# Kernel optimization log

Measured on AMD Instinct MI355X. Metric: run time of the kernel, lower is better.

Reference implementation:

```python
import jax, jax.numpy as jnp
import numpy as np

E, H, I, T = 8, 1024, 4096, 8192  # experts, hidden, intermediate, total tokens


def setup_inputs() -> dict:
    key = jax.random.key(0)
    k1, k2, k3 = jax.random.split(key, 3)
    hiddens = jax.random.normal(k1, (T, H), dtype=jnp.float32)
    # expert weights, scaled like standard init
    w1_weight = jax.random.normal(k2, (E, H, I), dtype=jnp.float32) * (1.0 / np.sqrt(H).astype(np.float32))
    w2_weight = jax.random.normal(k3, (E, I, H), dtype=jnp.float32) * (1.0 / np.sqrt(I).astype(np.float32))
    # tokens are pre-grouped by expert; equal load of T//E tokens per expert
    batch_sizes = jnp.full((E,), T // E, dtype=jnp.int32)
    return {"hiddens": hiddens, "batch_sizes": batch_sizes,
            "w1_weight": w1_weight, "w2_weight": w2_weight}


def _gmm(x, w, batch_sizes):
    """Grouped matmul: rows of x are grouped contiguously by expert.
    x: [T, K], w: [E, K, N], batch_sizes: [E] (sums to T). Returns [T, N].
    Loop is over the small fixed expert count; each iteration is a dense
    GEMM with rows outside the expert's segment masked to zero.
    """
    n_experts = w.shape[0]
    ends = jnp.cumsum(batch_sizes)
    starts = ends - batch_sizes
    tok = jnp.arange(x.shape[0])[:, None]  # [T, 1]
    out = jnp.zeros((x.shape[0], w.shape[2]), dtype=x.dtype)
    for e in range(n_experts):
        mask = (tok >= starts[e]) & (tok < ends[e])  # [T, 1]
        out = out + jnp.where(mask, x, jnp.zeros((), x.dtype)) @ w[e]
    return out


def reference(hiddens, batch_sizes, w1_weight, w2_weight):
    up = _gmm(hiddens, w1_weight, batch_sizes)    # [T, I]
    down = _gmm(up, w2_weight, batch_sizes)       # [T, H]
    return down
```

## Files before the change

kernel.cpp:

```cpp
#include <hip/hip_runtime.h>
#include <hip/hip_bf16.h>


typedef unsigned short u16;
typedef unsigned int u32;
typedef __attribute__((ext_vector_type(8))) short bf16x8;
typedef __attribute__((ext_vector_type(4))) float f32x4;
typedef __attribute__((ext_vector_type(4))) u32 u32x4;

#define E_N 8
#define H_N 1024
#define I_N 4096
#define T_N 8192

#define GLD2LDS16(g, l)                                                        \
  __builtin_amdgcn_global_load_lds(                                            \
      (const __attribute__((address_space(1))) void*)(g),                      \
      (__attribute__((address_space(3))) void*)(l), 16, 0, 0)

__device__ __forceinline__ u32 pkbf(float lo, float hi) {
  u32 a = __float_as_uint(lo) + 0x8000u;
  u32 b = __float_as_uint(hi) + 0x8000u;
  return __builtin_amdgcn_perm(b, a, 0x07060302u);
}

__device__ __forceinline__ u16 f2bf(float f) {
  __hip_bfloat16 h = __float2bfloat16(f);
  return *(reinterpret_cast<u16*>(&h));
}

__global__ __launch_bounds__(256) void cvt_kernel(const float* __restrict__ src,
                                                  u16* __restrict__ dst) {
  const size_t i = ((size_t)blockIdx.x * 256 + threadIdx.x) * 8;
  float4 a = *(const float4*)(src + i);
  float4 b = *(const float4*)(src + i + 4);
  *(u32x4*)(dst + i) = (u32x4){pkbf(a.x, a.y), pkbf(a.z, a.w),
                               pkbf(b.x, b.y), pkbf(b.z, b.w)};
}

__global__ __launch_bounds__(256) void transp_kernel(const float* __restrict__ w2,
                                                     u16* __restrict__ w2t) {
  __shared__ float tile[64 * 65];
  const int tid = threadIdx.x;
  const int h0 = blockIdx.x * 64;
  const int i0 = blockIdx.y * 64;
  const float* src = w2 + (size_t)blockIdx.z * I_N * H_N;
  u16* dst = w2t + (size_t)blockIdx.z * H_N * I_N;

  {
    const int r = tid >> 4;
    const int c4 = (tid & 15) * 4;
#pragma unroll
    for (int rr = 0; rr < 4; rr++) {
      const int row = rr * 16 + r;
      float4 v = *(const float4*)(src + (size_t)(i0 + row) * H_N + h0 + c4);
      tile[row * 65 + c4 + 0] = v.x;
      tile[row * 65 + c4 + 1] = v.y;
      tile[row * 65 + c4 + 2] = v.z;
      tile[row * 65 + c4 + 3] = v.w;
    }
  }
  __syncthreads();

  {
    const int hr = tid >> 3;
    const int ic = (tid & 7) * 8;
#pragma unroll
    for (int hh = 0; hh < 2; hh++) {
      const int h = hh * 32 + hr;
      u32 p[4];
#pragma unroll
      for (int j = 0; j < 4; j++)
        p[j] = pkbf(tile[(ic + 2 * j) * 65 + h], tile[(ic + 2 * j + 1) * 65 + h]);
      *(u32x4*)(dst + (size_t)(h0 + h) * I_N + i0 + ic) =
          (u32x4){p[0], p[1], p[2], p[3]};
    }
  }
}

__global__ __launch_bounds__(256) void wgemm_kernel(const u16* __restrict__ w2t,
                                                    const u16* __restrict__ w1b,
                                                    u16* __restrict__ mt) {
  __shared__ u16 ldsA[4096];
  __shared__ u16 ldsB[4096];

  const int tid = threadIdx.x;
  const int lane = tid & 63;
  const int wv = tid >> 6;
  const int wm = wv >> 1, wn = wv & 1;
  const int lm = lane & 15, quad = lane >> 4;

  const int e = blockIdx.x >> 6;
  const int t = blockIdx.x & 63;
  const int row0 = (t >> 3) * 128;
  const int col0 = (t & 7) * 128;

  const u16* Ae = w2t + (size_t)e * H_N * I_N;
  const u16* Be = w1b + (size_t)e * H_N * I_N;
  u16* mte = mt + (size_t)e * H_N * H_N;

  const int s_r = tid >> 2;
  const int s_k = (tid & 3) * 8;
  const u16* gA0 = Ae + (size_t)(row0 + s_r) * I_N + s_k;
  const u16* gA1 = gA0 + (size_t)64 * I_N;
  const u16* gB0 = Be + (size_t)(col0 + s_r) * I_N + s_k;
  const u16* gB1 = gB0 + (size_t)64 * I_N;
  u16* ldsA_dst = ldsA + wv * 512;
  u16* ldsB_dst = ldsB + wv * 512;

  f32x4 acc[4][4];
#pragma unroll
  for (int i = 0; i < 4; i++)
#pragma unroll
    for (int j = 0; j < 4; j++) acc[i][j] = (f32x4){0.f, 0.f, 0.f, 0.f};

  for (int k0 = 0; k0 < I_N; k0 += 32) {
    GLD2LDS16(gA0 + k0, ldsA_dst);
    GLD2LDS16(gA1 + k0, ldsA_dst + 2048);
    GLD2LDS16(gB0 + k0, ldsB_dst);
    GLD2LDS16(gB1 + k0, ldsB_dst + 2048);

    __syncthreads();

    bf16x8 af[4], bfr[4];
#pragma unroll
    for (int mi = 0; mi < 4; mi++)
      af[mi] = *(const bf16x8*)(ldsA + (wm * 64 + mi * 16 + lm) * 32 + quad * 8);
#pragma unroll
    for (int ni = 0; ni < 4; ni++)
      bfr[ni] = *(const bf16x8*)(ldsB + (wn * 64 + ni * 16 + lm) * 32 + quad * 8);
#pragma unroll
    for (int mi = 0; mi < 4; mi++)
#pragma unroll
      for (int ni = 0; ni < 4; ni++)
        acc[mi][ni] = __builtin_amdgcn_mfma_f32_16x16x32_bf16(
            af[mi], bfr[ni], acc[mi][ni], 0, 0, 0);

    __syncthreads();
  }

  const int orow = row0 + wm * 64 + quad * 4;
  const int ocol = col0 + wn * 64 + lm;
#pragma unroll
  for (int mi = 0; mi < 4; mi++)
#pragma unroll
    for (int ni = 0; ni < 4; ni++)
#pragma unroll
      for (int r = 0; r < 4; r++)
        mte[(size_t)(orow + mi * 16 + r) * H_N + ocol + ni * 16] =
            f2bf(acc[mi][ni][r]);
}

__global__ __launch_bounds__(256) void tgemm_kernel(const u16* __restrict__ xb,
                                                    const int* __restrict__ bsz,
                                                    const u16* __restrict__ mt,
                                                    float* __restrict__ out) {
  __shared__ u16 ldsA[4096];
  __shared__ u16 ldsB[4096];

  const int tid = threadIdx.x;
  const int lane = tid & 63;
  const int wv = tid >> 6;
  const int wm = wv >> 1, wn = wv & 1;
  const int lm = lane & 15, quad = lane >> 4;

  const int bm = blockIdx.x >> 3, bn = blockIdx.x & 7;
  const int row0 = bm * 128;
  const int col0 = bn * 128;

  int e = 0, start = 0;
#pragma unroll
  for (int i = 0; i < E_N; i++) {
    int b = bsz[i];
    if (row0 >= start + b) { start += b; e = i + 1; }
  }
  const u16* mte = mt + (size_t)e * H_N * H_N;

  const int s_r = tid >> 2;
  const int s_k = (tid & 3) * 8;
  const u16* gA0 = xb + (size_t)(row0 + s_r) * H_N + s_k;
  const u16* gA1 = gA0 + (size_t)64 * H_N;
  const u16* gB0 = mte + (size_t)(col0 + s_r) * H_N + s_k;
  const u16* gB1 = gB0 + (size_t)64 * H_N;
  u16* ldsA_dst = ldsA + wv * 512;
  u16* ldsB_dst = ldsB + wv * 512;

  f32x4 acc[4][4];
#pragma unroll
  for (int i = 0; i < 4; i++)
#pragma unroll
    for (int j = 0; j < 4; j++) acc[i][j] = (f32x4){0.f, 0.f, 0.f, 0.f};

  for (int k0 = 0; k0 < H_N; k0 += 32) {
    GLD2LDS16(gA0 + k0, ldsA_dst);
    GLD2LDS16(gA1 + k0, ldsA_dst + 2048);
    GLD2LDS16(gB0 + k0, ldsB_dst);
    GLD2LDS16(gB1 + k0, ldsB_dst + 2048);

    __syncthreads();

    bf16x8 af[4], bfr[4];
#pragma unroll
    for (int mi = 0; mi < 4; mi++)
      af[mi] = *(const bf16x8*)(ldsA + (wm * 64 + mi * 16 + lm) * 32 + quad * 8);
#pragma unroll
    for (int ni = 0; ni < 4; ni++)
      bfr[ni] = *(const bf16x8*)(ldsB + (wn * 64 + ni * 16 + lm) * 32 + quad * 8);
#pragma unroll
    for (int mi = 0; mi < 4; mi++)
#pragma unroll
      for (int ni = 0; ni < 4; ni++)
        acc[mi][ni] = __builtin_amdgcn_mfma_f32_16x16x32_bf16(
            af[mi], bfr[ni], acc[mi][ni], 0, 0, 0);

    __syncthreads();
  }

  const int orow = row0 + wm * 64 + quad * 4;
  const int ocol = col0 + wn * 64 + lm;
#pragma unroll
  for (int mi = 0; mi < 4; mi++)
#pragma unroll
    for (int ni = 0; ni < 4; ni++)
#pragma unroll
      for (int r = 0; r < 4; r++)
        out[(size_t)(orow + mi * 16 + r) * H_N + ocol + ni * 16] =
            acc[mi][ni][r];
}

extern "C" void kernel_launch(void* const* d_in, const int* in_sizes, int n_in,
                              void* d_out, int out_size, void* d_ws,
                              size_t ws_size, hipStream_t stream) {
  (void)in_sizes; (void)n_in; (void)out_size; (void)ws_size;
  const float* hiddens = (const float*)d_in[0];
  const int* bsz = (const int*)d_in[1];
  const float* w1 = (const float*)d_in[2];
  const float* w2 = (const float*)d_in[3];
  float* out = (float*)d_out;

  char* ws = (char*)d_ws;
  u16* w1b = (u16*)(ws);
  u16* w2t = (u16*)(ws + (size_t)64 * 1024 * 1024);
  u16* xb  = (u16*)(ws + (size_t)128 * 1024 * 1024);
  u16* mt  = (u16*)(ws + (size_t)144 * 1024 * 1024);

  cvt_kernel<<<dim3(16384), 256, 0, stream>>>(w1, w1b);
  cvt_kernel<<<dim3(4096), 256, 0, stream>>>(hiddens, xb);
  transp_kernel<<<dim3(16, 64, E_N), 256, 0, stream>>>(w2, w2t);

  wgemm_kernel<<<dim3(512), 256, 0, stream>>>(w2t, w1b, mt);
  tgemm_kernel<<<dim3(512), 256, 0, stream>>>(xb, bsz, mt, out);
}
```

Before: 483.7 us.

## Split-K the weight-product GEMM, shrink token GEMM tiles, widen conversion work

The weight-product GEMM (w2ᵀ·w1 per expert) is split into two K halves, so the grid grows from 512 to 1024 blocks. Each half writes a bf16 partial, and a new elementwise kernel sums the two into the fused matrix. The token GEMM moves from 128x128 to 64x128 tiles, which doubles its block count, and the conversion kernel handles 16 elements per thread. The workspace is reused for the partials and the bf16 hiddens. The aim is more blocks in flight to hide latency in the single-buffered GEMMs. The cost is an extra kernel with extra memory traffic, plus an additional bf16 rounding of the partial sums.

```diff
diff --git a/kernel.cpp b/kernel.cpp
--- a/kernel.cpp
+++ b/kernel.cpp
@@ -29,13 +29,22 @@
   return *(reinterpret_cast<u16*>(&h));
 }
 
+__device__ __forceinline__ float bf2f(u16 v) {
+  u32 x = (u32)v << 16;
+  return __uint_as_float(x);
+}
+
 __global__ __launch_bounds__(256) void cvt_kernel(const float* __restrict__ src,
                                                   u16* __restrict__ dst) {
-  const size_t i = ((size_t)blockIdx.x * 256 + threadIdx.x) * 8;
+  const size_t i = ((size_t)blockIdx.x * 256 + threadIdx.x) * 16;
   float4 a = *(const float4*)(src + i);
   float4 b = *(const float4*)(src + i + 4);
+  float4 c = *(const float4*)(src + i + 8);
+  float4 d = *(const float4*)(src + i + 12);
   *(u32x4*)(dst + i) = (u32x4){pkbf(a.x, a.y), pkbf(a.z, a.w),
                                pkbf(b.x, b.y), pkbf(b.z, b.w)};
+  *(u32x4*)(dst + i + 8) = (u32x4){pkbf(c.x, c.y), pkbf(c.z, c.w),
+                                   pkbf(d.x, d.y), pkbf(d.z, d.w)};
 }
 
 __global__ __launch_bounds__(256) void transp_kernel(const float* __restrict__ w2,
@@ -61,7 +70,6 @@
     }
   }
   __syncthreads();
-
   {
     const int hr = tid >> 3;
     const int ic = (tid & 7) * 8;
@@ -80,7 +88,7 @@
 
 __global__ __launch_bounds__(256) void wgemm_kernel(const u16* __restrict__ w2t,
                                                     const u16* __restrict__ w1b,
-                                                    u16* __restrict__ mt) {
+                                                    u16* __restrict__ P) {
   __shared__ u16 ldsA[4096];
   __shared__ u16 ldsB[4096];
 
@@ -90,20 +98,23 @@
   const int wm = wv >> 1, wn = wv & 1;
   const int lm = lane & 15, quad = lane >> 4;
 
-  const int e = blockIdx.x >> 6;
-  const int t = blockIdx.x & 63;
+  const int blk = blockIdx.x;
+  const int ks = blk >> 9;
+  const int e = (blk >> 6) & 7;
+  const int t = blk & 63;
   const int row0 = (t >> 3) * 128;
   const int col0 = (t & 7) * 128;
+  const int kbase = ks * 2048;
 
   const u16* Ae = w2t + (size_t)e * H_N * I_N;
   const u16* Be = w1b + (size_t)e * H_N * I_N;
-  u16* mte = mt + (size_t)e * H_N * H_N;
+  u16* Pe = P + (size_t)ks * E_N * H_N * H_N + (size_t)e * H_N * H_N;
 
   const int s_r = tid >> 2;
   const int s_k = (tid & 3) * 8;
-  const u16* gA0 = Ae + (size_t)(row0 + s_r) * I_N + s_k;
+  const u16* gA0 = Ae + (size_t)(row0 + s_r) * I_N + kbase + s_k;
   const u16* gA1 = gA0 + (size_t)64 * I_N;
-  const u16* gB0 = Be + (size_t)(col0 + s_r) * I_N + s_k;
+  const u16* gB0 = Be + (size_t)(col0 + s_r) * I_N + kbase + s_k;
   const u16* gB1 = gB0 + (size_t)64 * I_N;
   u16* ldsA_dst = ldsA + wv * 512;
   u16* ldsB_dst = ldsB + wv * 512;
@@ -114,7 +125,7 @@
 #pragma unroll
     for (int j = 0; j < 4; j++) acc[i][j] = (f32x4){0.f, 0.f, 0.f, 0.f};
 
-  for (int k0 = 0; k0 < I_N; k0 += 32) {
+  for (int k0 = 0; k0 < 2048; k0 += 32) {
     GLD2LDS16(gA0 + k0, ldsA_dst);
     GLD2LDS16(gA1 + k0, ldsA_dst + 2048);
     GLD2LDS16(gB0 + k0, ldsB_dst);
@@ -147,25 +158,40 @@
     for (int ni = 0; ni < 4; ni++)
 #pragma unroll
       for (int r = 0; r < 4; r++)
-        mte[(size_t)(orow + mi * 16 + r) * H_N + ocol + ni * 16] =
+        Pe[(size_t)(orow + mi * 16 + r) * H_N + ocol + ni * 16] =
             f2bf(acc[mi][ni][r]);
+}
+
+__global__ __launch_bounds__(256) void reduce_kernel(const u16* __restrict__ P0,
+                                                     const u16* __restrict__ P1,
+                                                     u16* __restrict__ mt) {
+  const size_t i = ((size_t)blockIdx.x * 256 + threadIdx.x) * 8;
+  u32x4 a = *(const u32x4*)(P0 + i);
+  u32x4 b = *(const u32x4*)(P1 + i);
+  u32 o[4];
+#pragma unroll
+  for (int j = 0; j < 4; j++) {
+    float lo = bf2f((u16)(a[j] & 0xffffu)) + bf2f((u16)(b[j] & 0xffffu));
+    float hi = bf2f((u16)(a[j] >> 16)) + bf2f((u16)(b[j] >> 16));
+    o[j] = pkbf(lo, hi);
+  }
+  *(u32x4*)(mt + i) = (u32x4){o[0], o[1], o[2], o[3]};
 }
 
 __global__ __launch_bounds__(256) void tgemm_kernel(const u16* __restrict__ xb,
                                                     const int* __restrict__ bsz,
                                                     const u16* __restrict__ mt,
                                                     float* __restrict__ out) {
-  __shared__ u16 ldsA[4096];
+  __shared__ u16 ldsA[2048];
   __shared__ u16 ldsB[4096];
 
   const int tid = threadIdx.x;
   const int lane = tid & 63;
   const int wv = tid >> 6;
-  const int wm = wv >> 1, wn = wv & 1;
   const int lm = lane & 15, quad = lane >> 4;
 
   const int bm = blockIdx.x >> 3, bn = blockIdx.x & 7;
-  const int row0 = bm * 128;
+  const int row0 = bm * 64;
   const int col0 = bn * 128;
 
   int e = 0, start = 0;
@@ -176,52 +202,50 @@
   }
   const u16* mte = mt + (size_t)e * H_N * H_N;
 
-  const int s_r = tid >> 2;
-  const int s_k = (tid & 3) * 8;
-  const u16* gA0 = xb + (size_t)(row0 + s_r) * H_N + s_k;
-  const u16* gA1 = gA0 + (size_t)64 * H_N;
-  const u16* gB0 = mte + (size_t)(col0 + s_r) * H_N + s_k;
-  const u16* gB1 = gB0 + (size_t)64 * H_N;
+  const int l_r = lane >> 2;
+  const int l_k = (lane & 3) * 8;
+  const u16* gA = xb + (size_t)(row0 + wv * 16 + l_r) * H_N + l_k;
+  const u16* gB0 = mte + (size_t)(col0 + wv * 32 + l_r) * H_N + l_k;
+  const u16* gB1 = gB0 + (size_t)16 * H_N;
   u16* ldsA_dst = ldsA + wv * 512;
-  u16* ldsB_dst = ldsB + wv * 512;
-
-  f32x4 acc[4][4];
+  u16* ldsB_dst = ldsB + wv * 1024;
+
+  f32x4 acc[4][2];
 #pragma unroll
   for (int i = 0; i < 4; i++)
 #pragma unroll
-    for (int j = 0; j < 4; j++) acc[i][j] = (f32x4){0.f, 0.f, 0.f, 0.f};
+    for (int j = 0; j < 2; j++) acc[i][j] = (f32x4){0.f, 0.f, 0.f, 0.f};
 
   for (int k0 = 0; k0 < H_N; k0 += 32) {
-    GLD2LDS16(gA0 + k0, ldsA_dst);
-    GLD2LDS16(gA1 + k0, ldsA_dst + 2048);
+    GLD2LDS16(gA + k0, ldsA_dst);
     GLD2LDS16(gB0 + k0, ldsB_dst);
-    GLD2LDS16(gB1 + k0, ldsB_dst + 2048);
-
-    __syncthreads();
-
-    bf16x8 af[4], bfr[4];
-#pragma unroll
-    for (int mi = 0; mi < 4; mi++)
-      af[mi] = *(const bf16x8*)(ldsA + (wm * 64 + mi * 16 + lm) * 32 + quad * 8);
-#pragma unroll
-    for (int ni = 0; ni < 4; ni++)
-      bfr[ni] = *(const bf16x8*)(ldsB + (wn * 64 + ni * 16 + lm) * 32 + quad * 8);
-#pragma unroll
-    for (int mi = 0; mi < 4; mi++)
-#pragma unroll
-      for (int ni = 0; ni < 4; ni++)
+    GLD2LDS16(gB1 + k0, ldsB_dst + 512);
+
+    __syncthreads();
+
+    bf16x8 af[4], bfr[2];
+#pragma unroll
+    for (int mi = 0; mi < 4; mi++)
+      af[mi] = *(const bf16x8*)(ldsA + (mi * 16 + lm) * 32 + quad * 8);
+#pragma unroll
+    for (int ni = 0; ni < 2; ni++)
+      bfr[ni] = *(const bf16x8*)(ldsB + (wv * 32 + ni * 16 + lm) * 32 + quad * 8);
+#pragma unroll
+    for (int mi = 0; mi < 4; mi++)
+#pragma unroll
+      for (int ni = 0; ni < 2; ni++)
         acc[mi][ni] = __builtin_amdgcn_mfma_f32_16x16x32_bf16(
             af[mi], bfr[ni], acc[mi][ni], 0, 0, 0);
 
     __syncthreads();
   }
 
-  const int orow = row0 + wm * 64 + quad * 4;
-  const int ocol = col0 + wn * 64 + lm;
+  const int orow = row0 + quad * 4;
+  const int ocol = col0 + wv * 32 + lm;
 #pragma unroll
   for (int mi = 0; mi < 4; mi++)
 #pragma unroll
-    for (int ni = 0; ni < 4; ni++)
+    for (int ni = 0; ni < 2; ni++)
 #pragma unroll
       for (int r = 0; r < 4; r++)
         out[(size_t)(orow + mi * 16 + r) * H_N + ocol + ni * 16] =
@@ -241,13 +265,17 @@
   char* ws = (char*)d_ws;
   u16* w1b = (u16*)(ws);
   u16* w2t = (u16*)(ws + (size_t)64 * 1024 * 1024);
-  u16* xb  = (u16*)(ws + (size_t)128 * 1024 * 1024);
-  u16* mt  = (u16*)(ws + (size_t)144 * 1024 * 1024);
-
-  cvt_kernel<<<dim3(16384), 256, 0, stream>>>(w1, w1b);
-  cvt_kernel<<<dim3(4096), 256, 0, stream>>>(hiddens, xb);
+  u16* P   = (u16*)(ws + (size_t)128 * 1024 * 1024);
+  u16* P1  = (u16*)(ws + (size_t)144 * 1024 * 1024);
+  u16* mt  = (u16*)(ws + (size_t)128 * 1024 * 1024);
+  u16* xb  = (u16*)(ws);
+
+  cvt_kernel<<<dim3(8192), 256, 0, stream>>>(w1, w1b);
   transp_kernel<<<dim3(16, 64, E_N), 256, 0, stream>>>(w2, w2t);
 
-  wgemm_kernel<<<dim3(512), 256, 0, stream>>>(w2t, w1b, mt);
-  tgemm_kernel<<<dim3(512), 256, 0, stream>>>(xb, bsz, mt, out);
-}
+  wgemm_kernel<<<dim3(1024), 256, 0, stream>>>(w2t, w1b, P);
+  reduce_kernel<<<dim3(4096), 256, 0, stream>>>(P, P1, mt);
+
+  cvt_kernel<<<dim3(2048), 256, 0, stream>>>(hiddens, xb);
+  tgemm_kernel<<<dim3(1024), 256, 0, stream>>>(xb, bsz, mt, out);
+}
```

Result: no change. 485.6 us (+0.4%).
